# Kernel optimization log

Measured on AMD Instinct MI355X. Metric: run time of the kernel, lower is better.

## Reference

```python
import jax, jax.numpy as jnp
import numpy as np

B, S, F = 8, 2048, 1024
NEG = -1000000000.0

def setup_inputs() -> dict:
    key = jax.random.key(0)
    ks = jax.random.split(key, 8)
    x = jax.random.normal(ks[0], (B, S, F), dtype=jnp.float32)
    # causal attention mask [S, S], 1 = keep, 0 = masked
    attn_mask = jnp.tril(jnp.ones((S, S), dtype=jnp.int32))
    # key padding mask [B, 1, S], random 0/1
    pad_mask = jax.random.randint(ks[1], (B, 1, S), 0, 2, dtype=jnp.int32)
    # ensure at least the first key position is valid per batch to avoid all-masked rows
    pad_mask = pad_mask.at[:, :, 0].set(1)
    sc = 1.0 / np.sqrt(F).astype(np.float32)
    Wq = jax.random.normal(ks[2], (F, F), dtype=jnp.float32) * sc
    bq = jax.random.normal(ks[3], (F,), dtype=jnp.float32) * 0.01
    Wk = jax.random.normal(ks[4], (F, F), dtype=jnp.float32) * sc
    bk = jax.random.normal(ks[5], (F,), dtype=jnp.float32) * 0.01
    Wv = jax.random.normal(ks[6], (F, F), dtype=jnp.float32) * sc
    bv = jax.random.normal(ks[7], (F,), dtype=jnp.float32) * 0.01
    return {"x": x, "attn_mask": attn_mask, "pad_mask": pad_mask,
            "Wq": Wq, "bq": bq, "Wk": Wk, "bk": bk, "Wv": Wv, "bv": bv}

def reference(x, attn_mask, pad_mask, Wq, bq, Wk, bk, Wv, bv):
    # torch Linear: y = x @ W.T + b
    q = jnp.einsum('bsf,of->bso', x, Wq) + bq
    k = jnp.einsum('bsf,of->bso', x, Wk) + bk
    v = jnp.einsum('bsf,of->bso', x, Wv) + bv
    scale = 1.0 / jnp.sqrt(jnp.asarray(q.shape[-1], dtype=x.dtype))
    scores = jnp.einsum('bqf,bkf->bqk', q, k) * scale  # [B, S, S]
    scores = jnp.where(pad_mask == 0, NEG, scores)            # pad_mask [B,1,S] broadcasts
    scores = jnp.where(attn_mask[None, :, :] == 0, NEG, scores)
    prob = jax.nn.softmax(scores, axis=-1)
    # dropout=0.0 (eval / identity)
    return jnp.einsum('bqk,bkf->bqf', prob, v)
```

## Files before the change

kernel.cpp:

```cpp
#include <hip/hip_runtime.h>
#include <hip/hip_bf16.h>
#include <stdint.h>


#define S_LEN 2048
#define F_DIM 1024
#define NBATCH 8
#define BS_TOT (NBATCH * S_LEN)

typedef __attribute__((ext_vector_type(8))) short bf16x8;
typedef __attribute__((ext_vector_type(4))) float f32x4;
typedef unsigned short u16;

__device__ __forceinline__ u16 f32_to_bf16_rne(float f) {
    union { float f; uint32_t u; } v; v.f = f;
    uint32_t u = v.u;
    u += 0x7FFFu + ((u >> 16) & 1u);
    return (u16)(u >> 16);
}
__device__ __forceinline__ float bf16_to_f32(u16 h) {
    union { uint32_t u; float f; } v; v.u = ((uint32_t)h) << 16;
    return v.f;
}

__device__ __forceinline__ void gload_lds16(const u16* g, u16* l) {
    __builtin_amdgcn_global_load_lds(
        (const __attribute__((address_space(1))) void*)g,
        (__attribute__((address_space(3))) void*)l,
        16, 0, 0);
}

__global__ __launch_bounds__(256) void cvt_f32_bf16(const float* __restrict__ in,
                                                    u16* __restrict__ out, int n) {
    int i = (blockIdx.x * 256 + threadIdx.x) * 4;
    if (i + 3 < n) {
        float4 f = *(const float4*)(in + i);
        ushort4 o;
        o.x = f32_to_bf16_rne(f.x); o.y = f32_to_bf16_rne(f.y);
        o.z = f32_to_bf16_rne(f.z); o.w = f32_to_bf16_rne(f.w);
        *(ushort4*)(out + i) = o;
    }
}

__global__ __launch_bounds__(256) void cvt_w3(const float* __restrict__ Wq,
                                              const float* __restrict__ Wk,
                                              const float* __restrict__ Wv,
                                              u16* __restrict__ Wb) {
    const int which = blockIdx.y;
    const float* in = (which == 0) ? Wq : (which == 1) ? Wk : Wv;
    int i = (blockIdx.x * 256 + threadIdx.x) * 4;
    float4 f = *(const float4*)(in + i);
    ushort4 o;
    o.x = f32_to_bf16_rne(f.x); o.y = f32_to_bf16_rne(f.y);
    o.z = f32_to_bf16_rne(f.z); o.w = f32_to_bf16_rne(f.w);
    *(ushort4*)(Wb + (size_t)which * F_DIM * F_DIM + i) = o;
}

template<class Epi>
__device__ __forceinline__ void gemm_tile_128(
    const u16* __restrict__ A, int lda,
    const u16* __restrict__ Bt, int ldb,
    int m0, int n0, int K, float alpha, Epi epi)
{
    __shared__ u16 la[128 * 32];
    __shared__ u16 lb[128 * 32];

    const int tid  = threadIdx.x;
    const int lane = tid & 63;
    const int wave = tid >> 6;
    const int wm = (wave & 1) * 64;
    const int wn = (wave >> 1) * 64;

    f32x4 acc[4][4];
#pragma unroll
    for (int mt = 0; mt < 4; mt++)
#pragma unroll
        for (int nt = 0; nt < 4; nt++)
            acc[mt][nt] = f32x4{0.f, 0.f, 0.f, 0.f};

    const int mrow = wm + (lane & 15);
    const int nrow = wn + (lane & 15);
    const int koff = (lane >> 4) * 8;

    const int cb0 = wave * 64;
    const int cb1 = wave * 64 + 256;
    const int lrow = lane >> 2;
    const int lcol = (lane & 3) * 8;
    const u16* pa0 = A  + (size_t)(m0 + (cb0 >> 2) + lrow) * lda + lcol;
    const u16* pa1 = A  + (size_t)(m0 + (cb1 >> 2) + lrow) * lda + lcol;
    const u16* pb0 = Bt + (size_t)(n0 + (cb0 >> 2) + lrow) * ldb + lcol;
    const u16* pb1 = Bt + (size_t)(n0 + (cb1 >> 2) + lrow) * ldb + lcol;
    u16* qa0 = la + cb0 * 8;
    u16* qa1 = la + cb1 * 8;
    u16* qb0 = lb + cb0 * 8;
    u16* qb1 = lb + cb1 * 8;

    for (int kk = 0; kk < K; kk += 32) {
        __syncthreads();
        gload_lds16(pa0 + kk, qa0);
        gload_lds16(pa1 + kk, qa1);
        gload_lds16(pb0 + kk, qb0);
        gload_lds16(pb1 + kk, qb1);
        __syncthreads();

        bf16x8 fa[4], fb[4];
#pragma unroll
        for (int t = 0; t < 4; t++) {
            fa[t] = *(const bf16x8*)(la + (mrow + t * 16) * 32 + koff);
            fb[t] = *(const bf16x8*)(lb + (nrow + t * 16) * 32 + koff);
        }
#pragma unroll
        for (int mt = 0; mt < 4; mt++)
#pragma unroll
            for (int nt = 0; nt < 4; nt++)
                acc[mt][nt] = __builtin_amdgcn_mfma_f32_16x16x32_bf16(
                    fa[mt], fb[nt], acc[mt][nt], 0, 0, 0);
    }

    const int col   = lane & 15;
    const int rquad = (lane >> 4) * 4;
#pragma unroll
    for (int mt = 0; mt < 4; mt++)
#pragma unroll
        for (int nt = 0; nt < 4; nt++) {
            const int n = n0 + wn + nt * 16 + col;
#pragma unroll
            for (int r = 0; r < 4; r++) {
                const int m = m0 + wm + mt * 16 + rquad + r;
                epi(m, n, acc[mt][nt][r] * alpha);
            }
        }
}

__global__ __launch_bounds__(256) void k_qkv(const u16* __restrict__ xb,
                                             const u16* __restrict__ Wb,
                                             const float* __restrict__ bq,
                                             const float* __restrict__ bk,
                                             const float* __restrict__ bv,
                                             u16* __restrict__ q,
                                             u16* __restrict__ k,
                                             u16* __restrict__ vT) {
    const int which = blockIdx.y;
    const int bx = blockIdx.x;
    const int xcd = bx & 7;
    const int idx = bx >> 3;
    const int m0 = (xcd * 16 + (idx >> 3)) * 128;
    const int n0 = (idx & 7) * 128;
    const float* bias = (which == 0) ? bq : (which == 1) ? bk : bv;
    const u16* W = Wb + (size_t)which * F_DIM * F_DIM;
    if (which < 2) {
        u16* o = (which == 0) ? q : k;
        gemm_tile_128(xb, F_DIM, W, F_DIM, m0, n0, F_DIM, 1.0f,
            [&](int m, int n, float v) {
                o[(size_t)m * F_DIM + n] = f32_to_bf16_rne(v + bias[n]);
            });
    } else {
        gemm_tile_128(xb, F_DIM, W, F_DIM, m0, n0, F_DIM, 1.0f,
            [&](int m, int n, float v) {
                vT[((size_t)(m >> 11) * F_DIM + n) * S_LEN + (m & 2047)] =
                    f32_to_bf16_rne(v + bias[n]);
            });
    }
}

__global__ __launch_bounds__(256) void k_scores(const u16* __restrict__ q,
                                                const u16* __restrict__ k,
                                                const int* __restrict__ pad,
                                                u16* __restrict__ Pp,
                                                float* __restrict__ lsum) {
    const int b = blockIdx.x & 7;
    const int t = blockIdx.x >> 3;
    int it = 0, base = 0;
    while (base + it + 1 <= t) { base += it + 1; it++; }
    const int jt = t - base;
    const int* padb = pad + b * S_LEN;
    u16* Pb = Pp + (size_t)b * S_LEN * S_LEN;

    float rs[16];
#pragma unroll
    for (int i = 0; i < 16; i++) rs[i] = 0.f;

    gemm_tile_128(q + (size_t)b * S_LEN * F_DIM, F_DIM,
                  k + (size_t)b * S_LEN * F_DIM, F_DIM,
                  it * 128, jt * 128, F_DIM, 0.03125f,
        [&](int m, int n, float v) {
            u16 o = 0;
            if (n <= m && padb[n] != 0)
                o = f32_to_bf16_rne(__expf(v - 16.0f));
            Pb[(size_t)m * S_LEN + n] = o;
            const int i = m & 63;
            rs[((i >> 4) << 2) | (i & 3)] += bf16_to_f32(o);
        });

    const int lane  = threadIdx.x & 63;
    const int wave  = threadIdx.x >> 6;
    const int wm    = (wave & 1) * 64;
    const int rquad = (lane >> 4) * 4;
    float* lb = lsum + b * S_LEN + it * 128 + wm;
#pragma unroll
    for (int i = 0; i < 16; i++) {
        float s = rs[i];
        s += __shfl_xor(s, 1);
        s += __shfl_xor(s, 2);
        s += __shfl_xor(s, 4);
        s += __shfl_xor(s, 8);
        if ((lane & 15) == 0)
            atomicAdd(&lb[((i >> 2) << 4) + rquad + (i & 3)], s);
    }
}

__global__ __launch_bounds__(256) void k_pv(const u16* __restrict__ Pp,
                                            const u16* __restrict__ vT,
                                            const float* __restrict__ lsum,
                                            float* __restrict__ out) {
    const int b = blockIdx.x & 7;
    const int rest = blockIdx.x >> 3;
    const int j = rest >> 3;
    const int nt = rest & 7;
    const int it = (j & 1) ? (j >> 1) : (15 - (j >> 1));
    const int Keff = (it + 1) * 128;
    const float* ls = lsum + b * S_LEN;
    float* ob = out + (size_t)b * S_LEN * F_DIM;

    const int lane  = threadIdx.x & 63;
    const int wave  = threadIdx.x >> 6;
    const int wm    = (wave & 1) * 64;
    const int rquad = (lane >> 4) * 4;
    const int mb    = it * 128 + wm;
    float myinv[16];
#pragma unroll
    for (int i = 0; i < 16; i++)
        myinv[i] = 1.0f / ls[mb + ((i >> 2) << 4) + rquad + (i & 3)];

    gemm_tile_128(Pp + (size_t)b * S_LEN * S_LEN, S_LEN,
                  vT + (size_t)b * F_DIM * S_LEN, S_LEN,
                  it * 128, nt * 128, Keff, 1.0f,
        [&](int m, int n, float v) {
            const int i = m & 63;
            ob[(size_t)m * F_DIM + n] = v * myinv[((i >> 4) << 2) | (i & 3)];
        });
}

extern "C" void kernel_launch(void* const* d_in, const int* in_sizes, int n_in,
                              void* d_out, int out_size, void* d_ws, size_t ws_size,
                              hipStream_t stream) {
    const float* x  = (const float*)d_in[0];
    const int* pad  = (const int*)d_in[2];
    const float* Wq = (const float*)d_in[3];
    const float* bq = (const float*)d_in[4];
    const float* Wk = (const float*)d_in[5];
    const float* bk = (const float*)d_in[6];
    const float* Wv = (const float*)d_in[7];
    const float* bv = (const float*)d_in[8];
    float* out = (float*)d_out;

    char* ws = (char*)d_ws;
    u16* q    = (u16*)(ws);
    u16* k    = (u16*)(ws + 32ull * 1024 * 1024);
    u16* vT   = (u16*)(ws + 64ull * 1024 * 1024);
    u16* Pp   = (u16*)(ws + 96ull * 1024 * 1024);
    u16* xb   = (u16*)(ws + 160ull * 1024 * 1024);
    u16* Wb   = (u16*)(ws + 192ull * 1024 * 1024);
    float* il = (float*)(ws + 200ull * 1024 * 1024);

    const int BSF = BS_TOT * F_DIM;
    const int FF = F_DIM * F_DIM;

    hipMemsetAsync(il, 0, BS_TOT * sizeof(float), stream);

    cvt_f32_bf16<<<BSF / 1024, 256, 0, stream>>>(x, xb, BSF);
    cvt_w3<<<dim3(FF / 1024, 3), 256, 0, stream>>>(Wq, Wk, Wv, Wb);

    k_qkv<<<dim3(1024, 3), 256, 0, stream>>>(xb, Wb, bq, bk, bv, q, k, vT);

    k_scores<<<1088, 256, 0, stream>>>(q, k, pad, Pp, il);

    k_pv<<<1024, 256, 0, stream>>>(Pp, vT, il, out);
}
```

Before: 407.0 us.

## Double-buffer LDS tiles in GEMM to overlap global loads with MFMA

Splits the shared-memory A/B tiles into two buffers and issues the next K-slice's global-to-LDS loads before computing on the current slice, halving the barriers per step. This aims to hide global load latency behind the MFMA work. It doubles LDS use per block, which may lower occupancy, and it assumes nsteps is even. The async LDS loads still rely on the barrier for completion, so the overlap depends on how the compiler places the waitcnt instructions.

```diff
diff --git a/kernel.cpp b/kernel.cpp
--- a/kernel.cpp
+++ b/kernel.cpp
@@ -62,8 +62,8 @@
     const u16* __restrict__ Bt, int ldb,
     int m0, int n0, int K, float alpha, Epi epi)
 {
-    __shared__ u16 la[128 * 32];
-    __shared__ u16 lb[128 * 32];
+    __shared__ u16 la[2][128 * 32];
+    __shared__ u16 lb[2][128 * 32];
 
     const int tid  = threadIdx.x;
     const int lane = tid & 63;
@@ -90,24 +90,19 @@
     const u16* pa1 = A  + (size_t)(m0 + (cb1 >> 2) + lrow) * lda + lcol;
     const u16* pb0 = Bt + (size_t)(n0 + (cb0 >> 2) + lrow) * ldb + lcol;
     const u16* pb1 = Bt + (size_t)(n0 + (cb1 >> 2) + lrow) * ldb + lcol;
-    u16* qa0 = la + cb0 * 8;
-    u16* qa1 = la + cb1 * 8;
-    u16* qb0 = lb + cb0 * 8;
-    u16* qb1 = lb + cb1 * 8;
-
-    for (int kk = 0; kk < K; kk += 32) {
-        __syncthreads();
-        gload_lds16(pa0 + kk, qa0);
-        gload_lds16(pa1 + kk, qa1);
-        gload_lds16(pb0 + kk, qb0);
-        gload_lds16(pb1 + kk, qb1);
-        __syncthreads();
-
+
+    auto STAGE = [&](u16* qa, u16* qb, int kk) {
+        gload_lds16(pa0 + kk, qa + cb0 * 8);
+        gload_lds16(pa1 + kk, qa + cb1 * 8);
+        gload_lds16(pb0 + kk, qb + cb0 * 8);
+        gload_lds16(pb1 + kk, qb + cb1 * 8);
+    };
+    auto COMPUTE = [&](const u16* La, const u16* Lb) {
         bf16x8 fa[4], fb[4];
 #pragma unroll
         for (int t = 0; t < 4; t++) {
-            fa[t] = *(const bf16x8*)(la + (mrow + t * 16) * 32 + koff);
-            fb[t] = *(const bf16x8*)(lb + (nrow + t * 16) * 32 + koff);
+            fa[t] = *(const bf16x8*)(La + (mrow + t * 16) * 32 + koff);
+            fb[t] = *(const bf16x8*)(Lb + (nrow + t * 16) * 32 + koff);
         }
 #pragma unroll
         for (int mt = 0; mt < 4; mt++)
@@ -115,6 +110,19 @@
             for (int nt = 0; nt < 4; nt++)
                 acc[mt][nt] = __builtin_amdgcn_mfma_f32_16x16x32_bf16(
                     fa[mt], fb[nt], acc[mt][nt], 0, 0, 0);
+    };
+
+    const int nsteps = K >> 5;
+
+    STAGE(la[0], lb[0], 0);
+    __syncthreads();
+    for (int s = 0; s < nsteps; s += 2) {
+        STAGE(la[1], lb[1], (s + 1) << 5);
+        COMPUTE(la[0], lb[0]);
+        __syncthreads();
+        if (s + 2 < nsteps) STAGE(la[0], lb[0], (s + 2) << 5);
+        COMPUTE(la[1], lb[1]);
+        __syncthreads();
     }
 
     const int col   = lane & 15;
```

Result: slower. 472.8 us (+16.2%).

## Compact unmasked keys per batch and skip fully padded score tiles

Applied to the files above, without the earlier changes.

Adds a prefix-scan kernel over the key padding mask that builds a compacted key index per batch and the number of valid keys needed by each query tile. The QKV epilogue now writes only unmasked K and V rows into compacted buffers. The score kernel skips tiles beyond the needed key count and uses the original positions for the causal test, and PV shortens its K loop to match. This removes roughly the masked fraction of the score and PV GEMM work, at the cost of scattered epilogue stores, an extra scan launch, and a memset of the compacted V buffer.

```diff
diff --git a/kernel.cpp b/kernel.cpp
--- a/kernel.cpp
+++ b/kernel.cpp
@@ -56,6 +56,42 @@
     *(ushort4*)(Wb + (size_t)which * F_DIM * F_DIM + i) = o;
 }
 
+__global__ __launch_bounds__(256) void k_scan(const int* __restrict__ pad,
+                                              int* __restrict__ cidx,
+                                              int* __restrict__ sIdx,
+                                              int* __restrict__ kneed) {
+    const int b = blockIdx.x;
+    const int tid = threadIdx.x;
+    const int* p = pad + b * S_LEN;
+    __shared__ int part[256];
+    __shared__ int cnt_s;
+    int v[8]; int sum = 0; const int s0 = tid * 8;
+#pragma unroll
+    for (int i = 0; i < 8; i++) { v[i] = p[s0 + i]; sum += v[i]; }
+    part[tid] = sum;
+    __syncthreads();
+    if (tid == 0) {
+        int acc = 0;
+        for (int i = 0; i < 256; i++) { int t = part[i]; part[i] = acc; acc += t; }
+        cnt_s = acc;
+    }
+    __syncthreads();
+    int run = part[tid];
+#pragma unroll
+    for (int i = 0; i < 8; i++) {
+        const int s = s0 + i;
+        cidx[b * S_LEN + s] = run;
+        if (v[i]) sIdx[b * S_LEN + run] = s;
+        run += v[i];
+    }
+    const int cnt = cnt_s;
+    for (int c = cnt + tid; c < S_LEN; c += 256) sIdx[b * S_LEN + c] = S_LEN;
+    if (tid < 16) {
+        const int et = (tid + 1) * 16 - 1;
+        kneed[b * 16 + tid] = (et == 255) ? cnt : part[et + 1];
+    }
+}
+
 template<class Epi>
 __device__ __forceinline__ void gemm_tile_128(
     const u16* __restrict__ A, int lda,
@@ -137,9 +173,11 @@
                                              const float* __restrict__ bq,
                                              const float* __restrict__ bk,
                                              const float* __restrict__ bv,
+                                             const int* __restrict__ pad,
+                                             const int* __restrict__ cidx,
                                              u16* __restrict__ q,
-                                             u16* __restrict__ k,
-                                             u16* __restrict__ vT) {
+                                             u16* __restrict__ kc,
+                                             u16* __restrict__ vTc) {
     const int which = blockIdx.y;
     const int bx = blockIdx.x;
     const int xcd = bx & 7;
@@ -148,24 +186,34 @@
     const int n0 = (idx & 7) * 128;
     const float* bias = (which == 0) ? bq : (which == 1) ? bk : bv;
     const u16* W = Wb + (size_t)which * F_DIM * F_DIM;
-    if (which < 2) {
-        u16* o = (which == 0) ? q : k;
+    if (which == 0) {
         gemm_tile_128(xb, F_DIM, W, F_DIM, m0, n0, F_DIM, 1.0f,
             [&](int m, int n, float v) {
-                o[(size_t)m * F_DIM + n] = f32_to_bf16_rne(v + bias[n]);
+                q[(size_t)m * F_DIM + n] = f32_to_bf16_rne(v + bias[n]);
+            });
+    } else if (which == 1) {
+        gemm_tile_128(xb, F_DIM, W, F_DIM, m0, n0, F_DIM, 1.0f,
+            [&](int m, int n, float v) {
+                const int b = m >> 11, s = m & 2047;
+                if (pad[b * S_LEN + s])
+                    kc[((size_t)b * S_LEN + cidx[b * S_LEN + s]) * F_DIM + n] =
+                        f32_to_bf16_rne(v + bias[n]);
             });
     } else {
         gemm_tile_128(xb, F_DIM, W, F_DIM, m0, n0, F_DIM, 1.0f,
             [&](int m, int n, float v) {
-                vT[((size_t)(m >> 11) * F_DIM + n) * S_LEN + (m & 2047)] =
-                    f32_to_bf16_rne(v + bias[n]);
+                const int b = m >> 11, s = m & 2047;
+                if (pad[b * S_LEN + s])
+                    vTc[((size_t)b * F_DIM + n) * S_LEN + cidx[b * S_LEN + s]] =
+                        f32_to_bf16_rne(v + bias[n]);
             });
     }
 }
 
 __global__ __launch_bounds__(256) void k_scores(const u16* __restrict__ q,
-                                                const u16* __restrict__ k,
-                                                const int* __restrict__ pad,
+                                                const u16* __restrict__ kc,
+                                                const int* __restrict__ sIdx,
+                                                const int* __restrict__ kneed,
                                                 u16* __restrict__ Pp,
                                                 float* __restrict__ lsum) {
     const int b = blockIdx.x & 7;
@@ -173,7 +221,8 @@
     int it = 0, base = 0;
     while (base + it + 1 <= t) { base += it + 1; it++; }
     const int jt = t - base;
-    const int* padb = pad + b * S_LEN;
+    if (jt * 128 >= kneed[b * 16 + it]) return;
+    const int* sIb = sIdx + b * S_LEN;
     u16* Pb = Pp + (size_t)b * S_LEN * S_LEN;
 
     float rs[16];
@@ -181,11 +230,11 @@
     for (int i = 0; i < 16; i++) rs[i] = 0.f;
 
     gemm_tile_128(q + (size_t)b * S_LEN * F_DIM, F_DIM,
-                  k + (size_t)b * S_LEN * F_DIM, F_DIM,
+                  kc + (size_t)b * S_LEN * F_DIM, F_DIM,
                   it * 128, jt * 128, F_DIM, 0.03125f,
         [&](int m, int n, float v) {
             u16 o = 0;
-            if (n <= m && padb[n] != 0)
+            if (sIb[n] <= m)
                 o = f32_to_bf16_rne(__expf(v - 16.0f));
             Pb[(size_t)m * S_LEN + n] = o;
             const int i = m & 63;
@@ -210,15 +259,16 @@
 }
 
 __global__ __launch_bounds__(256) void k_pv(const u16* __restrict__ Pp,
-                                            const u16* __restrict__ vT,
+                                            const u16* __restrict__ vTc,
                                             const float* __restrict__ lsum,
+                                            const int* __restrict__ kneed,
                                             float* __restrict__ out) {
     const int b = blockIdx.x & 7;
     const int rest = blockIdx.x >> 3;
     const int j = rest >> 3;
     const int nt = rest & 7;
     const int it = (j & 1) ? (j >> 1) : (15 - (j >> 1));
-    const int Keff = (it + 1) * 128;
+    const int Keff = (kneed[b * 16 + it] + 127) & ~127;
     const float* ls = lsum + b * S_LEN;
     float* ob = out + (size_t)b * S_LEN * F_DIM;
 
@@ -233,7 +283,7 @@
         myinv[i] = 1.0f / ls[mb + ((i >> 2) << 4) + rquad + (i & 3)];
 
     gemm_tile_128(Pp + (size_t)b * S_LEN * S_LEN, S_LEN,
-                  vT + (size_t)b * F_DIM * S_LEN, S_LEN,
+                  vTc + (size_t)b * F_DIM * S_LEN, S_LEN,
                   it * 128, nt * 128, Keff, 1.0f,
         [&](int m, int n, float v) {
             const int i = m & 63;
@@ -256,24 +306,30 @@
 
     char* ws = (char*)d_ws;
     u16* q    = (u16*)(ws);
-    u16* k    = (u16*)(ws + 32ull * 1024 * 1024);
-    u16* vT   = (u16*)(ws + 64ull * 1024 * 1024);
+    u16* kc   = (u16*)(ws + 32ull * 1024 * 1024);
+    u16* vTc  = (u16*)(ws + 64ull * 1024 * 1024);
     u16* Pp   = (u16*)(ws + 96ull * 1024 * 1024);
     u16* xb   = (u16*)(ws + 160ull * 1024 * 1024);
     u16* Wb   = (u16*)(ws + 192ull * 1024 * 1024);
     float* il = (float*)(ws + 200ull * 1024 * 1024);
+    int* cidx = (int*)(ws + 201ull * 1024 * 1024);
+    int* sIdx = (int*)(ws + 202ull * 1024 * 1024);
+    int* kneed= (int*)(ws + 203ull * 1024 * 1024);
 
     const int BSF = BS_TOT * F_DIM;
     const int FF = F_DIM * F_DIM;
 
     hipMemsetAsync(il, 0, BS_TOT * sizeof(float), stream);
+    hipMemsetAsync(vTc, 0, 32ull * 1024 * 1024, stream);
 
     cvt_f32_bf16<<<BSF / 1024, 256, 0, stream>>>(x, xb, BSF);
     cvt_w3<<<dim3(FF / 1024, 3), 256, 0, stream>>>(Wq, Wk, Wv, Wb);
-
-    k_qkv<<<dim3(1024, 3), 256, 0, stream>>>(xb, Wb, bq, bk, bv, q, k, vT);
-
-    k_scores<<<1088, 256, 0, stream>>>(q, k, pad, Pp, il);
-
-    k_pv<<<1024, 256, 0, stream>>>(Pp, vT, il, out);
-}
+    k_scan<<<NBATCH, 256, 0, stream>>>(pad, cidx, sIdx, kneed);
+
+    k_qkv<<<dim3(1024, 3), 256, 0, stream>>>(xb, Wb, bq, bk, bv, pad, cidx,
+                                             q, kc, vTc);
+
+    k_scores<<<1088, 256, 0, stream>>>(q, kc, sIdx, kneed, Pp, il);
+
+    k_pv<<<1024, 256, 0, stream>>>(Pp, vTc, il, kneed, out);
+}
```

New measurement: 386.5 us. 5.0% less time.
